# Kernel optimization log

Measured on AMD Instinct MI355X. Metric: run time of the kernel, lower is better.

## Reference

```python
import jax, jax.numpy as jnp
import numpy as np

B, C, M, N = 256, 8, 16, 4096
R, D = 64, 64  # len(r_target), len(d_target); N == R * D


def setup_inputs() -> dict:
    key = jax.random.key(0)
    k1, k2, k3, k4 = jax.random.split(key, 4)
    x = jax.random.normal(k1, (B, C, M, N), dtype=jnp.float32)
    # Conv2d weight: [out_channels=1, in_channels=C, kH=M, kW=1]
    W = jax.random.normal(k2, (1, C, M, 1), dtype=jnp.float32) * 0.1
    r_target = jax.random.normal(k3, (R,), dtype=jnp.float32)
    d_target = jax.random.normal(k4, (D,), dtype=jnp.float32)
    return {"input_feature": x, "W": W, "r_target": r_target, "d_target": d_target}


def reference(input_feature, W, r_target, d_target):
    # Conv2d with kernel (M,1), out_channels=1, no bias: contracts channel and
    # M dims -> [B, 1, 1, N], then squeeze -> [B, N]
    outputs = jnp.einsum('bcmn,cm->bn', input_feature, W[0, :, :, 0])

    index = jnp.argmax(outputs, axis=1)  # [B]

    len_r = r_target.shape[0]
    len_d = d_target.shape[0]
    # Faithful to original: div by len(r_target), multiply back by len(d_target)
    r_index = index // len_r
    d_index = index - (index // len_r) * len_d

    # Original assigns float values into int64 ones_like(index) tensors,
    # which truncates toward zero; replicate that cast.
    r = r_target[r_index].astype(index.dtype)
    d = d_target[d_index].astype(index.dtype)

    output = (r, d)
    return (outputs, d, output)
```

## Files before the change

### kernel.cpp

```cpp
#include <hip/hip_runtime.h>


#define BATCH   256
#define NDIM    4096
#define CM      128
#define THREADS 1024
#define NWAVES  (THREADS / 64)
#define GROUP   8
#define NGROUPS (CM / GROUP)

typedef float v4f __attribute__((ext_vector_type(4)));

__global__ __launch_bounds__(THREADS, 4) void conv_argmax_kernel(
    const float* __restrict__ x, const float* __restrict__ W,
    const float* __restrict__ r_target, const float* __restrict__ d_target,
    float* __restrict__ out)
{
    __shared__ float w[CM];
    __shared__ float sval[NWAVES];
    __shared__ int   sidx[NWAVES];

    const int b   = blockIdx.x;
    const int tid = threadIdx.x;

    if (tid < CM) w[tid] = W[tid];
    __syncthreads();

    const int n0 = tid * 4;
    const float* xp = x + (size_t)b * (CM * NDIM) + n0;

    float acc0 = 0.f, acc1 = 0.f, acc2 = 0.f, acc3 = 0.f;

    #pragma unroll
    for (int g = 0; g < NGROUPS; ++g) {
        v4f v[GROUP];
        #pragma unroll
        for (int j = 0; j < GROUP; ++j) {
            v[j] = __builtin_nontemporal_load(
                (const v4f*)(xp + (size_t)(g * GROUP + j) * NDIM));
        }
        #pragma unroll
        for (int j = 0; j < GROUP; ++j) {
            const float wc = w[g * GROUP + j];
            acc0 += v[j].x * wc;
            acc1 += v[j].y * wc;
            acc2 += v[j].z * wc;
            acc3 += v[j].w * wc;
        }
    }

    v4f o;
    o.x = acc0; o.y = acc1; o.z = acc2; o.w = acc3;
    __builtin_nontemporal_store(o, (v4f*)(out + (size_t)b * NDIM + n0));

    float bv = acc0; int bi = n0;
    if (acc1 > bv) { bv = acc1; bi = n0 + 1; }
    if (acc2 > bv) { bv = acc2; bi = n0 + 2; }
    if (acc3 > bv) { bv = acc3; bi = n0 + 3; }

    for (int off = 32; off >= 1; off >>= 1) {
        float ov = __shfl_down(bv, off, 64);
        int   oi = __shfl_down(bi, off, 64);
        if (ov > bv || (ov == bv && oi < bi)) { bv = ov; bi = oi; }
    }
    const int wave = tid >> 6;
    if ((tid & 63) == 0) { sval[wave] = bv; sidx[wave] = bi; }
    __syncthreads();

    if (tid == 0) {
        #pragma unroll
        for (int i = 1; i < NWAVES; ++i) {
            if (sval[i] > bv || (sval[i] == bv && sidx[i] < bi)) {
                bv = sval[i]; bi = sidx[i];
            }
        }
        const int r_index = bi >> 6;
        const int d_index = bi & 63;
        const float r = (float)(int)r_target[r_index];
        const float d = (float)(int)d_target[d_index];
        const int BN = BATCH * NDIM;
        out[BN + b]             = d;
        out[BN + BATCH + b]     = r;
        out[BN + 2 * BATCH + b] = d;
    }
}

extern "C" void kernel_launch(void* const* d_in, const int* in_sizes, int n_in,
                              void* d_out, int out_size, void* d_ws, size_t ws_size,
                              hipStream_t stream) {
    const float* x        = (const float*)d_in[0];
    const float* W        = (const float*)d_in[1];
    const float* r_target = (const float*)d_in[2];
    const float* d_target = (const float*)d_in[3];
    float* out = (float*)d_out;

    conv_argmax_kernel<<<BATCH, THREADS, 0, stream>>>(x, W, r_target, d_target, out);
}
```

Baseline: 646.0 us.

## Split each batch row across four blocks with a separate argmax finalize kernel

```diff
diff --git a/kernel.cpp b/kernel.cpp
--- a/kernel.cpp
+++ b/kernel.cpp
@@ -4,34 +4,37 @@
 #define BATCH   256
 #define NDIM    4096
 #define CM      128
-#define THREADS 1024
-#define NWAVES  (THREADS / 64)
+#define SLICES  4
+#define SLICE_COLS (NDIM / SLICES)
+#define THREADS1   (SLICE_COLS / 4)
+#define NWAVES1    (THREADS1 / 64)
 #define GROUP   8
 #define NGROUPS (CM / GROUP)
 
 typedef float v4f __attribute__((ext_vector_type(4)));
 
-__global__ __launch_bounds__(THREADS, 4) void conv_argmax_kernel(
+__global__ __launch_bounds__(THREADS1) void conv_partial_kernel(
     const float* __restrict__ x, const float* __restrict__ W,
-    const float* __restrict__ r_target, const float* __restrict__ d_target,
-    float* __restrict__ out)
+    float* __restrict__ out, float2* __restrict__ partial)
 {
     __shared__ float w[CM];
-    __shared__ float sval[NWAVES];
-    __shared__ int   sidx[NWAVES];
+    __shared__ float sval[NWAVES1];
+    __shared__ int   sidx[NWAVES1];
 
-    const int b   = blockIdx.x;
+    const int blk = blockIdx.x;
+    const int b   = blk >> 2;
+    const int s   = blk & (SLICES - 1);
     const int tid = threadIdx.x;
 
     if (tid < CM) w[tid] = W[tid];
     __syncthreads();
 
-    const int n0 = tid * 4;
+    const int n0 = s * SLICE_COLS + tid * 4;
     const float* xp = x + (size_t)b * (CM * NDIM) + n0;
 
     float acc0 = 0.f, acc1 = 0.f, acc2 = 0.f, acc3 = 0.f;
 
-    #pragma unroll
+    #pragma unroll 1
     for (int g = 0; g < NGROUPS; ++g) {
         v4f v[GROUP];
         #pragma unroll
@@ -69,20 +72,38 @@
 
     if (tid == 0) {
         #pragma unroll
-        for (int i = 1; i < NWAVES; ++i) {
+        for (int i = 1; i < NWAVES1; ++i) {
             if (sval[i] > bv || (sval[i] == bv && sidx[i] < bi)) {
                 bv = sval[i]; bi = sidx[i];
             }
         }
-        const int r_index = bi >> 6;
-        const int d_index = bi & 63;
-        const float r = (float)(int)r_target[r_index];
-        const float d = (float)(int)d_target[d_index];
-        const int BN = BATCH * NDIM;
-        out[BN + b]             = d;
-        out[BN + BATCH + b]     = r;
-        out[BN + 2 * BATCH + b] = d;
+        partial[blk] = make_float2(bv, __int_as_float(bi));
     }
+}
+
+__global__ __launch_bounds__(256) void finalize_kernel(
+    const float2* __restrict__ partial,
+    const float* __restrict__ r_target, const float* __restrict__ d_target,
+    float* __restrict__ out)
+{
+    const int b = threadIdx.x;
+    float2 p = partial[b * SLICES];
+    float bv = p.x;
+    int   bi = __float_as_int(p.y);
+    #pragma unroll
+    for (int s = 1; s < SLICES; ++s) {
+        float2 q = partial[b * SLICES + s];
+        const int qi = __float_as_int(q.y);
+        if (q.x > bv || (q.x == bv && qi < bi)) { bv = q.x; bi = qi; }
+    }
+    const int r_index = bi >> 6;
+    const int d_index = bi & 63;
+    const float r = (float)(int)r_target[r_index];
+    const float d = (float)(int)d_target[d_index];
+    const int BN = BATCH * NDIM;
+    out[BN + b]             = d;
+    out[BN + BATCH + b]     = r;
+    out[BN + 2 * BATCH + b] = d;
 }
 
 extern "C" void kernel_launch(void* const* d_in, const int* in_sizes, int n_in,
@@ -93,6 +114,8 @@
     const float* r_target = (const float*)d_in[2];
     const float* d_target = (const float*)d_in[3];
     float* out = (float*)d_out;
+    float2* partial = (float2*)d_ws;
 
-    conv_argmax_kernel<<<BATCH, THREADS, 0, stream>>>(x, W, r_target, d_target, out);
+    conv_partial_kernel<<<BATCH * SLICES, THREADS1, 0, stream>>>(x, W, out, partial);
+    finalize_kernel<<<1, 256, 0, stream>>>(partial, r_target, d_target, out);
 }
```

New measurement: 670.6 us. 3.8% more time.
